# Optimization experiments

Measured on AMD Instinct MI355X. Metric: run time of the kernel, lower is better.

The kernel has to match this reference:

```python
import jax, jax.numpy as jnp
import numpy as np

NHEAD = 8

def setup_inputs() -> dict:
    key = jax.random.key(0)
    ks = jax.random.split(key, 7)
    B, N, D = 8, 1024, 512
    scale = 1.0 / np.sqrt(D)
    return {
        "x": jax.random.normal(ks[0], (B, N, D), dtype=jnp.float32),
        "graph_bias": jax.random.normal(ks[1], (B, N, N), dtype=jnp.float32),
        "in_proj_w": jax.random.normal(ks[2], (3 * D, D), dtype=jnp.float32) * scale,
        "in_proj_b": jax.random.normal(ks[3], (3 * D,), dtype=jnp.float32) * 0.02,
        "out_proj_w": jax.random.normal(ks[4], (D, D), dtype=jnp.float32) * scale,
        "out_proj_b": jax.random.normal(ks[5], (D,), dtype=jnp.float32) * 0.02,
        "bias_strength": jnp.ones((), dtype=jnp.float32),
    }

def reference(x, graph_bias, in_proj_w, in_proj_b, out_proj_w, out_proj_b, bias_strength):
    B, N, D = x.shape
    H = NHEAD
    hd = D // H
    # fused QKV projection (matches nn.MultiheadAttention in_proj)
    qkv = x @ in_proj_w.T + in_proj_b          # (B, N, 3D)
    q, k, v = jnp.split(qkv, 3, axis=-1)
    # (B, H, N, hd)
    q = q.reshape(B, N, H, hd).transpose(0, 2, 1, 3)
    k = k.reshape(B, N, H, hd).transpose(0, 2, 1, 3)
    v = v.reshape(B, N, H, hd).transpose(0, 2, 1, 3)
    # additive bias from predicted causal structure
    alpha = jax.nn.sigmoid(bias_strength)
    causal_mask = jax.nn.sigmoid(graph_bias).transpose(0, 2, 1)   # (B, N, N)
    causal_mask = alpha * causal_mask + (1.0 - alpha) * 0.5
    attn_bias = (causal_mask - 0.5) * 10.0                        # (B, N, N)
    scores = jnp.einsum("bhqd,bhkd->bhqk", q, k) / jnp.sqrt(jnp.asarray(hd, x.dtype))
    scores = scores + attn_bias[:, None, :, :]                    # broadcast over heads
    probs = jax.nn.softmax(scores, axis=-1)
    out = jnp.einsum("bhqk,bhkd->bhqd", probs, v)                 # (B, H, N, hd)
    out = out.transpose(0, 2, 1, 3).reshape(B, N, D)
    return out @ out_proj_w.T + out_proj_b
```

## Files before the change

### kernel.cpp

```cpp
#include <hip/hip_runtime.h>

typedef __attribute__((ext_vector_type(8))) __bf16 bf16x8;
typedef __attribute__((ext_vector_type(4))) __bf16 bf16x4;
typedef __attribute__((ext_vector_type(4))) float f32x4;
typedef __attribute__((ext_vector_type(8))) _Float16 f16x8;

#define LOG2E 1.44269504088896340736f

__device__ __forceinline__ void async_load16(const void* g, void* l) {
  __builtin_amdgcn_global_load_lds(
      (const __attribute__((address_space(1))) void*)g,
      (__attribute__((address_space(3))) void*)l, 16, 0, 0);
}

__device__ __forceinline__ float fast_exp2(float x) {
#if __has_builtin(__builtin_amdgcn_exp2f)
  return __builtin_amdgcn_exp2f(x);
#else
  return __expf(x * 0.6931471805599453f);
#endif
}

__global__ void cvt3(const float* __restrict__ a, __bf16* __restrict__ oa, int na4,
                     const float* __restrict__ b, __bf16* __restrict__ ob, int nb4,
                     const float* __restrict__ c, __bf16* __restrict__ oc, int nc4) {
  int i = blockIdx.x * blockDim.x + threadIdx.x;
  int n = na4 + nb4 + nc4;
  int stride = gridDim.x * blockDim.x;
  for (; i < n; i += stride) {
    const float4* s;
    bf16x4* d;
    int j;
    if (i < na4) { s = (const float4*)a; d = (bf16x4*)oa; j = i; }
    else if (i < na4 + nb4) { s = (const float4*)b; d = (bf16x4*)ob; j = i - na4; }
    else { s = (const float4*)c; d = (bf16x4*)oc; j = i - na4 - nb4; }
    float4 v = s[j];
    bf16x4 o;
    o[0] = (__bf16)v.x; o[1] = (__bf16)v.y; o[2] = (__bf16)v.z; o[3] = (__bf16)v.w;
    d[j] = o;
  }
}

__global__ __launch_bounds__(256) void build_ebias(
    const float* __restrict__ gbias, const float* __restrict__ bstr,
    _Float16* __restrict__ ebT) {
  const int gid = blockIdx.x * 256 + threadIdx.x;
  const int lane = gid & 63;
  const int kt = (gid >> 6) & 31;
  const int qt = (gid >> 11) & 63;
  const int b = gid >> 17;
  const int g = lane >> 4, ln = lane & 15;
  const float alpha = 1.f / (1.f + __expf(-bstr[0]));
  const float bsc = 10.f * alpha * LOG2E;
  const float* base = gbias + (size_t)(b * 1024 + kt * 32 + ln) * 1024 + qt * 16 + g * 4;
  float4 va = *(const float4*)(base);
  float4 vb = *(const float4*)(base + 16 * 1024);
  float sv[8] = {va.x, va.y, va.z, va.w, vb.x, vb.y, vb.z, vb.w};
  f16x8 o;
#pragma unroll
  for (int i = 0; i < 8; ++i)
    o[i] = (_Float16)((1.f / (1.f + __expf(-sv[i])) - 0.5f) * bsc);
  *(f16x8*)(ebT + (size_t)gid * 8) = o;
}

template <int MODE>
__global__ __launch_bounds__(256) void gemm_bt(
    const __bf16* __restrict__ A, const __bf16* __restrict__ Bm,
    const float* __restrict__ bias, void* __restrict__ C0,
    __bf16* __restrict__ vT, int M, int N, int K) {
  __shared__ __align__(16) char smem[32768];
  char* lA = smem;
  char* lB = smem + 16384;
  const int t = threadIdx.x;
  const int lane = t & 63;
  const int wid = t >> 6;
  const int wm = wid >> 1, wn = wid & 1;
  const int g = lane >> 4, ln = lane & 15;
  const int m0 = blockIdx.y * 128;
  const int n0 = blockIdx.x * 128;

  const int srow = t >> 3;
  const int sswz = ((t & 7) * 16) ^ ((srow & 7) << 4);
  const size_t KB = (size_t)K * 2;
  const char* gA = (const char*)A + (size_t)m0 * KB;
  const char* gB = (const char*)Bm + (size_t)n0 * KB;

  f32x4 acc[4][4] = {};

  for (int k0 = 0; k0 < K; k0 += 64) {
    __syncthreads();
#pragma unroll
    for (int c = 0; c < 4; ++c) {
      int row = srow + 32 * c;
      async_load16(gA + (size_t)row * KB + k0 * 2 + sswz, lA + c * 4096 + t * 16);
      async_load16(gB + (size_t)row * KB + k0 * 2 + sswz, lB + c * 4096 + t * 16);
    }
    __syncthreads();
#pragma unroll
    for (int ks = 0; ks < 2; ++ks) {
      bf16x8 af[4], bf[4];
#pragma unroll
      for (int i = 0; i < 4; ++i) {
        int ar = wm * 64 + i * 16 + ln;
        int byo = (ks * 64 + g * 16) ^ ((ar & 7) << 4);
        af[i] = *(const bf16x8*)(lA + ar * 128 + byo);
        int br = wn * 64 + i * 16 + ln;
        bf[i] = *(const bf16x8*)(lB + br * 128 + byo);
      }
#pragma unroll
      for (int i = 0; i < 4; ++i)
#pragma unroll
        for (int j = 0; j < 4; ++j)
          acc[i][j] = __builtin_amdgcn_mfma_f32_16x16x32_bf16(af[i], bf[j], acc[i][j], 0, 0, 0);
    }
  }

#pragma unroll
  for (int j = 0; j < 4; ++j) {
    int col = n0 + wn * 64 + j * 16 + ln;
    float bv = bias[col];
    if (MODE == 0) {
#pragma unroll
      for (int i = 0; i < 4; ++i) {
        int row0 = m0 + wm * 64 + i * 16 + g * 4;
#pragma unroll
        for (int r = 0; r < 4; ++r)
          ((float*)C0)[(size_t)(row0 + r) * N + col] = acc[i][j][r] + bv;
      }
    } else if (col < 1024) {
      float scale = (col < 512) ? (0.125f * LOG2E) : 1.0f;
#pragma unroll
      for (int i = 0; i < 4; ++i) {
        int row0 = m0 + wm * 64 + i * 16 + g * 4;
#pragma unroll
        for (int r = 0; r < 4; ++r)
          ((__bf16*)C0)[(size_t)(row0 + r) * 1024 + col] = (__bf16)((acc[i][j][r] + bv) * scale);
      }
    } else {
      int h = (col - 1024) >> 6;
      int d = (col - 1024) & 63;
#pragma unroll
      for (int i = 0; i < 4; ++i) {
        int row0 = m0 + wm * 64 + i * 16 + g * 4;
        int b = row0 >> 10;
        bf16x4 pk;
#pragma unroll
        for (int r = 0; r < 4; ++r) pk[r] = (__bf16)(acc[i][j][r] + bv);
        *(bf16x4*)(vT + (((size_t)b * 8 + h) * 64 + d) * 1024 + (row0 & 1023)) = pk;
      }
    }
  }
}

__global__ __launch_bounds__(512, 4) void attn_fused(
    const __bf16* __restrict__ qk,
    const __bf16* __restrict__ vT,
    const _Float16* __restrict__ ebT,
    __bf16* __restrict__ attn) {
  __shared__ __align__(16) char smem[24576];
  const int t = threadIdx.x;
  const int lane = t & 63;
  const int wid = t >> 6;
  const int g = lane >> 4, ln = lane & 15;
  const int wg = ((blockIdx.x & 7) << 6) + (blockIdx.x >> 3);
  const int b = wg >> 6;
  const int rem = wg & 63;
  const int h = rem >> 3;
  const int qg = rem & 7;
  const int qt = qg * 8 + wid;
  const int q0 = qt << 4;

  char* K0 = smem;
  char* K1 = smem + 4096;
  char* V0 = smem + 8192;
  char* V1 = smem + 12288;
  char* Ps = smem + 16384 + wid * 1024;

  bf16x8 qf[2];
#pragma unroll
  for (int ks = 0; ks < 2; ++ks)
    qf[ks] = *(const bf16x8*)(qk + ((size_t)b * 1024 + q0 + ln) * 1024 +
                              h * 64 + ks * 32 + g * 8);

  float l_acc[4] = {0.f, 0.f, 0.f, 0.f};
  f32x4 o_acc[4] = {};

  const int krow = lane >> 3;
  const int ksrc = ((lane & 7) * 16) ^ (krow << 4);
  const int vrow = lane >> 2;
  const int vsrc = ((lane & 3) * 16) ^ ((vrow & 3) << 4);

  const char* qkb = (const char*)qk + (size_t)b * 1024 * 2048;
  const char* vTb = (const char*)vT + (size_t)(b * 8 + h) * 64 * 2048;
  const _Float16* ebp = ebT + (size_t)((b * 64 + qt) * 32) * 512 + lane * 8;

  auto stage = [&](int kt, char* Kd, char* Vd) {
    if (wid < 4) {
      async_load16(qkb + (size_t)(kt * 32 + wid * 8 + krow) * 2048 + 1024 + h * 128 + ksrc,
                   Kd + wid * 1024 + lane * 16);
    } else {
      int c = wid - 4;
      async_load16(vTb + (size_t)(c * 16 + vrow) * 2048 + (size_t)(kt * 32) * 2 + vsrc,
                   Vd + c * 1024 + lane * 16);
    }
  };

  stage(0, K0, V0);
  f16x8 ebc = *(const f16x8*)(ebp);
  asm volatile("s_waitcnt vmcnt(0)" ::: "memory");
  __syncthreads();

  for (int kt = 0; kt < 32; ++kt) {
    char* Kp = (kt & 1) ? K1 : K0;
    char* Vp = (kt & 1) ? V1 : V0;
    char* Kn = (kt & 1) ? K0 : K1;
    char* Vn = (kt & 1) ? V0 : V1;
    const int ktn = (kt + 1) & 31;

    stage(ktn, Kn, Vn);
    f16x8 ebn = *(const f16x8*)(ebp + (size_t)ktn * 512);
    __builtin_amdgcn_sched_barrier(0);

    bf16x8 kf[2][2];
#pragma unroll
    for (int ni = 0; ni < 2; ++ni) {
      int br = ni * 16 + ln;
      int sw = (br & 7) << 4;
#pragma unroll
      for (int ks = 0; ks < 2; ++ks)
        kf[ni][ks] = *(const bf16x8*)(Kp + br * 128 + ((ks * 64 + g * 16) ^ sw));
    }
    bf16x8 vf[4];
#pragma unroll
    for (int di = 0; di < 4; ++di)
      vf[di] = *(const bf16x8*)(Vp + (di * 16 + ln) * 64 + ((g * 16) ^ ((ln & 3) << 4)));

    f32x4 lbf0 = {(float)ebc[0], (float)ebc[1], (float)ebc[2], (float)ebc[3]};
    f32x4 lbf1 = {(float)ebc[4], (float)ebc[5], (float)ebc[6], (float)ebc[7]};
    f32x4 s[2];
    s[0] = __builtin_amdgcn_mfma_f32_16x16x32_bf16(qf[0], kf[0][0], lbf0, 0, 0, 0);
    s[0] = __builtin_amdgcn_mfma_f32_16x16x32_bf16(qf[1], kf[0][1], s[0], 0, 0, 0);
    s[1] = __builtin_amdgcn_mfma_f32_16x16x32_bf16(qf[0], kf[1][0], lbf1, 0, 0, 0);
    s[1] = __builtin_amdgcn_mfma_f32_16x16x32_bf16(qf[1], kf[1][1], s[1], 0, 0, 0);

#pragma unroll
    for (int r = 0; r < 4; ++r) {
      float p0 = fast_exp2(s[0][r]);
      float p1 = fast_exp2(s[1][r]);
      s[0][r] = p0; s[1][r] = p1;
      l_acc[r] += p0 + p1;
    }
#pragma unroll
    for (int ni = 0; ni < 2; ++ni)
#pragma unroll
      for (int r = 0; r < 4; ++r) {
        int q = g * 4 + r;
        *(__bf16*)(Ps + q * 64 + ((ni * 32 + ln * 2) ^ (((q >> 1) & 3) << 4))) =
            (__bf16)s[ni][r];
      }
    bf16x8 pf = *(const bf16x8*)(Ps + ln * 64 + ((g * 16) ^ (((ln >> 1) & 3) << 4)));

#pragma unroll
    for (int di = 0; di < 4; ++di)
      o_acc[di] = __builtin_amdgcn_mfma_f32_16x16x32_bf16(pf, vf[di], o_acc[di], 0, 0, 0);

    asm volatile("s_waitcnt vmcnt(0)" ::: "memory");
    __syncthreads();
    ebc = ebn;
  }

#pragma unroll
  for (int r = 0; r < 4; ++r) {
    float rs = l_acc[r];
#pragma unroll
    for (int off = 1; off < 16; off <<= 1)
      rs += __shfl_xor(rs, off, 64);
    float inv = 1.f / rs;
    int q = q0 + g * 4 + r;
#pragma unroll
    for (int di = 0; di < 4; ++di)
      attn[((size_t)b * 1024 + q) * 512 + h * 64 + di * 16 + ln] =
          (__bf16)(o_acc[di][r] * inv);
  }
}

extern "C" void kernel_launch(void* const* d_in, const int* in_sizes, int n_in,
                              void* d_out, int out_size, void* d_ws, size_t ws_size,
                              hipStream_t stream) {
  const float* x     = (const float*)d_in[0];
  const float* gb    = (const float*)d_in[1];
  const float* w_in  = (const float*)d_in[2];
  const float* b_in  = (const float*)d_in[3];
  const float* w_out = (const float*)d_in[4];
  const float* b_out = (const float*)d_in[5];
  const float* bstr  = (const float*)d_in[6];

  char* ws = (char*)d_ws;
  __bf16* qk    = (__bf16*)(ws);
  __bf16* vT    = (__bf16*)(ws + 16777216);
  __bf16* xb    = (__bf16*)(ws + 25165824);
  __bf16* w1    = (__bf16*)(ws + 33554432);
  __bf16* w2    = (__bf16*)(ws + 35127296);
  _Float16* ebT = (_Float16*)(ws + 35651584);
  __bf16* attn_buf = xb;

  cvt3<<<2560, 256, 0, stream>>>(x, xb, (8 * 1024 * 512) / 4,
                                 w_in, w1, (1536 * 512) / 4,
                                 w_out, w2, (512 * 512) / 4);
  build_ebias<<<4096, 256, 0, stream>>>(gb, bstr, ebT);

  gemm_bt<1><<<dim3(12, 64), 256, 0, stream>>>(xb, w1, b_in, qk, vT, 8192, 1536, 512);
  attn_fused<<<512, 512, 0, stream>>>(qk, vT, ebT, attn_buf);
  gemm_bt<0><<<dim3(4, 64), 256, 0, stream>>>(attn_buf, w2, b_out, d_out, nullptr, 8192, 512, 512);
}
```

Measured before the change: 96.63 us.

## Merge prep kernels and stage two KV tiles per barrier in attention

```diff
diff --git a/kernel.cpp b/kernel.cpp
--- a/kernel.cpp
+++ b/kernel.cpp
@@ -21,46 +21,47 @@
 #endif
 }
 
-__global__ void cvt3(const float* __restrict__ a, __bf16* __restrict__ oa, int na4,
-                     const float* __restrict__ b, __bf16* __restrict__ ob, int nb4,
-                     const float* __restrict__ c, __bf16* __restrict__ oc, int nc4) {
-  int i = blockIdx.x * blockDim.x + threadIdx.x;
-  int n = na4 + nb4 + nc4;
-  int stride = gridDim.x * blockDim.x;
-  for (; i < n; i += stride) {
-    const float4* s;
-    bf16x4* d;
-    int j;
-    if (i < na4) { s = (const float4*)a; d = (bf16x4*)oa; j = i; }
-    else if (i < na4 + nb4) { s = (const float4*)b; d = (bf16x4*)ob; j = i - na4; }
-    else { s = (const float4*)c; d = (bf16x4*)oc; j = i - na4 - nb4; }
-    float4 v = s[j];
-    bf16x4 o;
-    o[0] = (__bf16)v.x; o[1] = (__bf16)v.y; o[2] = (__bf16)v.z; o[3] = (__bf16)v.w;
-    d[j] = o;
-  }
-}
-
-__global__ __launch_bounds__(256) void build_ebias(
+__global__ __launch_bounds__(256) void prep(
     const float* __restrict__ gbias, const float* __restrict__ bstr,
-    _Float16* __restrict__ ebT) {
-  const int gid = blockIdx.x * 256 + threadIdx.x;
-  const int lane = gid & 63;
-  const int kt = (gid >> 6) & 31;
-  const int qt = (gid >> 11) & 63;
-  const int b = gid >> 17;
-  const int g = lane >> 4, ln = lane & 15;
-  const float alpha = 1.f / (1.f + __expf(-bstr[0]));
-  const float bsc = 10.f * alpha * LOG2E;
-  const float* base = gbias + (size_t)(b * 1024 + kt * 32 + ln) * 1024 + qt * 16 + g * 4;
-  float4 va = *(const float4*)(base);
-  float4 vb = *(const float4*)(base + 16 * 1024);
-  float sv[8] = {va.x, va.y, va.z, va.w, vb.x, vb.y, vb.z, vb.w};
-  f16x8 o;
-#pragma unroll
-  for (int i = 0; i < 8; ++i)
-    o[i] = (_Float16)((1.f / (1.f + __expf(-sv[i])) - 0.5f) * bsc);
-  *(f16x8*)(ebT + (size_t)gid * 8) = o;
+    _Float16* __restrict__ ebT,
+    const float* __restrict__ a, __bf16* __restrict__ oa, int na4,
+    const float* __restrict__ b2, __bf16* __restrict__ ob, int nb4,
+    const float* __restrict__ c, __bf16* __restrict__ oc, int nc4) {
+  if (blockIdx.x < 4096) {
+    const int gid = blockIdx.x * 256 + threadIdx.x;
+    const int lane = gid & 63;
+    const int kt = (gid >> 6) & 31;
+    const int qt = (gid >> 11) & 63;
+    const int b = gid >> 17;
+    const int g = lane >> 4, ln = lane & 15;
+    const float alpha = 1.f / (1.f + __expf(-bstr[0]));
+    const float bsc = 10.f * alpha * LOG2E;
+    const float* base = gbias + (size_t)(b * 1024 + kt * 32 + ln) * 1024 + qt * 16 + g * 4;
+    float4 va = *(const float4*)(base);
+    float4 vb = *(const float4*)(base + 16 * 1024);
+    float sv[8] = {va.x, va.y, va.z, va.w, vb.x, vb.y, vb.z, vb.w};
+    f16x8 o;
+#pragma unroll
+    for (int i = 0; i < 8; ++i)
+      o[i] = (_Float16)((1.f / (1.f + __expf(-sv[i])) - 0.5f) * bsc);
+    *(f16x8*)(ebT + (size_t)gid * 8) = o;
+  } else {
+    int i = (blockIdx.x - 4096) * 256 + threadIdx.x;
+    int n = na4 + nb4 + nc4;
+    int stride = 2560 * 256;
+    for (; i < n; i += stride) {
+      const float4* s;
+      bf16x4* d;
+      int j;
+      if (i < na4) { s = (const float4*)a; d = (bf16x4*)oa; j = i; }
+      else if (i < na4 + nb4) { s = (const float4*)b2; d = (bf16x4*)ob; j = i - na4; }
+      else { s = (const float4*)c; d = (bf16x4*)oc; j = i - na4 - nb4; }
+      float4 v = s[j];
+      bf16x4 o;
+      o[0] = (__bf16)v.x; o[1] = (__bf16)v.y; o[2] = (__bf16)v.z; o[3] = (__bf16)v.w;
+      d[j] = o;
+    }
+  }
 }
 
 template <int MODE>
@@ -157,7 +158,7 @@
     const __bf16* __restrict__ vT,
     const _Float16* __restrict__ ebT,
     __bf16* __restrict__ attn) {
-  __shared__ __align__(16) char smem[24576];
+  __shared__ __align__(16) char smem[40960];
   const int t = threadIdx.x;
   const int lane = t & 63;
   const int wid = t >> 6;
@@ -170,11 +171,7 @@
   const int qt = qg * 8 + wid;
   const int q0 = qt << 4;
 
-  char* K0 = smem;
-  char* K1 = smem + 4096;
-  char* V0 = smem + 8192;
-  char* V1 = smem + 12288;
-  char* Ps = smem + 16384 + wid * 1024;
+  char* Ps = smem + 32768 + wid * 1024;
 
   bf16x8 qf[2];
 #pragma unroll
@@ -194,33 +191,22 @@
   const char* vTb = (const char*)vT + (size_t)(b * 8 + h) * 64 * 2048;
   const _Float16* ebp = ebT + (size_t)((b * 64 + qt) * 32) * 512 + lane * 8;
 
-  auto stage = [&](int kt, char* Kd, char* Vd) {
+  auto stage = [&](int p, char* set) {
     if (wid < 4) {
-      async_load16(qkb + (size_t)(kt * 32 + wid * 8 + krow) * 2048 + 1024 + h * 128 + ksrc,
-                   Kd + wid * 1024 + lane * 16);
+      async_load16(qkb + (size_t)((2 * p) * 32 + wid * 8 + krow) * 2048 + 1024 + h * 128 + ksrc,
+                   set + wid * 1024 + lane * 16);
+      async_load16(qkb + (size_t)((2 * p + 1) * 32 + wid * 8 + krow) * 2048 + 1024 + h * 128 + ksrc,
+                   set + 4096 + wid * 1024 + lane * 16);
     } else {
-      int c = wid - 4;
-      async_load16(vTb + (size_t)(c * 16 + vrow) * 2048 + (size_t)(kt * 32) * 2 + vsrc,
-                   Vd + c * 1024 + lane * 16);
+      int cc = wid - 4;
+      async_load16(vTb + (size_t)(cc * 16 + vrow) * 2048 + (size_t)(2 * p) * 64 + vsrc,
+                   set + 8192 + cc * 1024 + lane * 16);
+      async_load16(vTb + (size_t)(cc * 16 + vrow) * 2048 + (size_t)(2 * p + 1) * 64 + vsrc,
+                   set + 12288 + cc * 1024 + lane * 16);
     }
   };
 
-  stage(0, K0, V0);
-  f16x8 ebc = *(const f16x8*)(ebp);
-  asm volatile("s_waitcnt vmcnt(0)" ::: "memory");
-  __syncthreads();
-
-  for (int kt = 0; kt < 32; ++kt) {
-    char* Kp = (kt & 1) ? K1 : K0;
-    char* Vp = (kt & 1) ? V1 : V0;
-    char* Kn = (kt & 1) ? K0 : K1;
-    char* Vn = (kt & 1) ? V0 : V1;
-    const int ktn = (kt + 1) & 31;
-
-    stage(ktn, Kn, Vn);
-    f16x8 ebn = *(const f16x8*)(ebp + (size_t)ktn * 512);
-    __builtin_amdgcn_sched_barrier(0);
-
+  auto process = [&](const char* Kp, const char* Vp, f16x8 ebv) {
     bf16x8 kf[2][2];
 #pragma unroll
     for (int ni = 0; ni < 2; ++ni) {
@@ -235,8 +221,8 @@
     for (int di = 0; di < 4; ++di)
       vf[di] = *(const bf16x8*)(Vp + (di * 16 + ln) * 64 + ((g * 16) ^ ((ln & 3) << 4)));
 
-    f32x4 lbf0 = {(float)ebc[0], (float)ebc[1], (float)ebc[2], (float)ebc[3]};
-    f32x4 lbf1 = {(float)ebc[4], (float)ebc[5], (float)ebc[6], (float)ebc[7]};
+    f32x4 lbf0 = {(float)ebv[0], (float)ebv[1], (float)ebv[2], (float)ebv[3]};
+    f32x4 lbf1 = {(float)ebv[4], (float)ebv[5], (float)ebv[6], (float)ebv[7]};
     f32x4 s[2];
     s[0] = __builtin_amdgcn_mfma_f32_16x16x32_bf16(qf[0], kf[0][0], lbf0, 0, 0, 0);
     s[0] = __builtin_amdgcn_mfma_f32_16x16x32_bf16(qf[1], kf[0][1], s[0], 0, 0, 0);
@@ -263,10 +249,32 @@
 #pragma unroll
     for (int di = 0; di < 4; ++di)
       o_acc[di] = __builtin_amdgcn_mfma_f32_16x16x32_bf16(pf, vf[di], o_acc[di], 0, 0, 0);
+  };
+
+  stage(0, smem);
+  f16x8 eba = *(const f16x8*)(ebp);
+  f16x8 ebb = *(const f16x8*)(ebp + 512);
+  asm volatile("s_waitcnt vmcnt(0)" ::: "memory");
+  __syncthreads();
+
+  for (int p = 0; p < 16; ++p) {
+    char* cur = smem + (p & 1) * 16384;
+    char* nxt = smem + ((p + 1) & 1) * 16384;
+    const int pn = (p + 1) & 15;
+
+    stage(pn, nxt);
+    f16x8 eba2 = *(const f16x8*)(ebp + (size_t)(2 * pn) * 512);
+    f16x8 ebb2 = *(const f16x8*)(ebp + (size_t)(2 * pn + 1) * 512);
+    __builtin_amdgcn_sched_barrier(0);
+
+    process(cur, cur + 8192, eba);
+    process(cur + 4096, cur + 12288, ebb);
 
     asm volatile("s_waitcnt vmcnt(0)" ::: "memory");
+    __builtin_amdgcn_sched_barrier(0);
     __syncthreads();
-    ebc = ebn;
+    eba = eba2;
+    ebb = ebb2;
   }
 
 #pragma unroll
@@ -304,10 +312,10 @@
   _Float16* ebT = (_Float16*)(ws + 35651584);
   __bf16* attn_buf = xb;
 
-  cvt3<<<2560, 256, 0, stream>>>(x, xb, (8 * 1024 * 512) / 4,
+  prep<<<6656, 256, 0, stream>>>(gb, bstr, ebT,
+                                 x, xb, (8 * 1024 * 512) / 4,
                                  w_in, w1, (1536 * 512) / 4,
                                  w_out, w2, (512 * 512) / 4);
-  build_ebias<<<4096, 256, 0, stream>>>(gb, bstr, ebT);
 
   gemm_bt<1><<<dim3(12, 64), 256, 0, stream>>>(xb, w1, b_in, qk, vT, 8192, 1536, 512);
   attn_fused<<<512, 512, 0, stream>>>(qk, vT, ebT, attn_buf);
```

Measured after the change: 90.32 us. -6.5%, faster.
